# Kernel optimization log

Measured on AMD Instinct MI355X. Metric: run time of the kernel, lower is better.

Reference implementation:

```python
import jax, jax.numpy as jnp
import numpy as np

B, C, H, W = 1024, 256, 19, 19
CH, CV = 32, 48  # c_head, c_val
B_AVG = 9.0


def setup_inputs() -> dict:
    key = jax.random.key(0)
    ks = jax.random.split(key, 14)
    s = 0.05
    d = {}
    d["x"] = jax.random.normal(ks[0], (B, C, H, W), jnp.float32)
    d["conv_w"] = jax.random.normal(ks[1], (CH, C), jnp.float32) * s  # 1x1 conv, no bias
    d["fc1_w"] = jax.random.normal(ks[2], (CV, 3 * CH), jnp.float32) * s
    d["fc1_b"] = jax.random.normal(ks[3], (CV,), jnp.float32) * s
    d["fc2_w"] = jax.random.normal(ks[4], (1, CV), jnp.float32) * s
    d["fc2_b"] = jax.random.normal(ks[5], (1,), jnp.float32) * s
    d["fc3_w"] = jax.random.normal(ks[6], (CV, 3 * CH), jnp.float32) * s
    d["fc3_b"] = jax.random.normal(ks[7], (CV,), jnp.float32) * s
    d["sc_w"] = jax.random.normal(ks[8], (1, CV), jnp.float32) * s
    d["sc_b"] = jax.random.normal(ks[9], (1,), jnp.float32) * s
    d["fc4_w"] = jax.random.normal(ks[10], (CV, 3 * CH + 1), jnp.float32) * s
    d["fc4_b"] = jax.random.normal(ks[11], (CV,), jnp.float32) * s
    d["fc5_w"] = jax.random.normal(ks[12], (1, CV), jnp.float32) * s
    d["fc5_b"] = jax.random.normal(ks[13], (1,), jnp.float32) * s
    return d


def reference(x, conv_w, fc1_w, fc1_b, fc2_w, fc2_b, fc3_w, fc3_b,
              sc_w, sc_b, fc4_w, fc4_b, fc5_w, fc5_b):
    # 1x1 conv (bias=False) == channel-mixing matmul
    V = jnp.einsum('bchw,oc->bohw', x, conv_w)  # [B, CH, H, W]

    # GlobalPooling (value_head=False branch: real spatial max)
    mean1 = V.mean(axis=(2, 3))                         # [B, CH]
    mean2 = mean1 * ((V.shape[2] - B_AVG) / 10.0)       # [B, CH]
    mx = V.max(axis=(2, 3))                             # [B, CH]
    Vp = jnp.concatenate([mean1, mean2, mx], axis=1)    # [B, 3*CH]

    # game outcome head
    game_out = jnp.tanh(jax.nn.relu(Vp @ fc1_w.T + fc1_b) @ fc2_w.T + fc2_b)  # [B, 1]

    # scaling factor head
    scaling = jax.nn.relu(Vp @ fc3_w.T + fc3_b) @ sc_w.T + sc_b  # [B, 1]

    # distance logits: the original loops over 41 d values; here the d axis is batched.
    dvals = jnp.arange(-20, 21, dtype=jnp.float32)               # [41]
    base = Vp @ fc4_w[:, :-1].T + fc4_b                          # [B, CV]
    d_term = dvals[:, None] * fc4_w[:, -1][None, :]              # [41, CV]
    h = jax.nn.relu(base[:, None, :] + d_term[None, :, :])       # [B, 41, CV]
    logits = h @ fc5_w[0] + fc5_b[0]                             # [B, 41]

    probs = jax.nn.softmax(logits * scaling, axis=1)             # [B, 41]
    return (game_out, probs)
```

## Files before the change

### kernel.cpp

```cpp
#include <hip/hip_runtime.h>
#include <math.h>

#define C_IN   256
#define C_HEAD 32
#define HW     361
#define NTHR   384
#define CV     48
#define WSTR   264

typedef __attribute__((ext_vector_type(8))) short bf16x8;
typedef __attribute__((ext_vector_type(4))) float f32x4;

static __device__ __forceinline__ unsigned short f2bf(float f) {
    unsigned int u = __builtin_bit_cast(unsigned int, f);
    u += 0x7fffu + ((u >> 16) & 1u);
    return (unsigned short)(u >> 16);
}

__global__ __launch_bounds__(NTHR, 4) void vh_fused(
    const float* __restrict__ x,
    const float* __restrict__ conv_w,
    const float* __restrict__ fc1_w, const float* __restrict__ fc1_b,
    const float* __restrict__ fc2_w, const float* __restrict__ fc2_b,
    const float* __restrict__ fc3_w, const float* __restrict__ fc3_b,
    const float* __restrict__ sc_w,  const float* __restrict__ sc_b,
    const float* __restrict__ fc4_w, const float* __restrict__ fc4_b,
    const float* __restrict__ fc5_w, const float* __restrict__ fc5_b,
    float* __restrict__ out, int B)
{
    const int b    = blockIdx.x;
    const int tid  = threadIdx.x;
    const int wave = tid >> 6;
    const int lane = tid & 63;
    const int l15  = lane & 15;
    const int g    = lane >> 4;

    __shared__ __align__(16) unsigned short wtT[C_HEAD * WSTR];
    __shared__ float lds_psum[C_HEAD][6];
    __shared__ float lds_pmax[C_HEAD][6];
    __shared__ float vp[3 * C_HEAD];
    __shared__ float base_l[CV], dco_l[CV], f5_l[CV];

    for (int i = tid; i < C_HEAD * C_IN; i += NTHR) {
        int o = i >> 8, c = i & 255;
        wtT[o * WSTR + c] = f2bf(conv_w[i]);
    }
    __syncthreads();

    f32x4 acc[4][2];
    #pragma unroll
    for (int mi = 0; mi < 4; ++mi)
        #pragma unroll
        for (int n = 0; n < 2; ++n)
            acc[mi][n] = (f32x4){0.f, 0.f, 0.f, 0.f};

    const float* __restrict__ xb = x + (size_t)b * C_IN * HW;

    #pragma unroll
    for (int t = 0; t < 8; ++t) {
        bf16x8 wf[2];
        #pragma unroll
        for (int n = 0; n < 2; ++n)
            wf[n] = *(const bf16x8*)&wtT[(n * 16 + l15) * WSTR + t * 32 + g * 8];

        bf16x8 a[4];
        #pragma unroll
        for (int mi = 0; mi < 4; ++mi) {
            int p = wave * 64 + mi * 16 + l15;
            if (p >= HW) p = HW - 1;
            const float* xp = xb + (t * 32 + g * 8) * HW + p;
            float v[8];
            #pragma unroll
            for (int e = 0; e < 8; ++e) v[e] = xp[e * HW];
            bf16x8 f;
            #pragma unroll
            for (int e = 0; e < 8; ++e) f[e] = (short)f2bf(v[e]);
            a[mi] = f;
        }

        #pragma unroll
        for (int mi = 0; mi < 4; ++mi)
            #pragma unroll
            for (int n = 0; n < 2; ++n)
                acc[mi][n] = __builtin_amdgcn_mfma_f32_16x16x32_bf16(
                    a[mi], wf[n], acc[mi][n], 0, 0, 0);
    }

    float s[2]  = {0.f, 0.f};
    float mx[2] = {-3.0e38f, -3.0e38f};
    #pragma unroll
    for (int n = 0; n < 2; ++n) {
        #pragma unroll
        for (int mi = 0; mi < 4; ++mi) {
            #pragma unroll
            for (int r = 0; r < 4; ++r) {
                int pp = wave * 64 + mi * 16 + g * 4 + r;
                float v = acc[mi][n][r];
                if (pp < HW) { s[n] += v; mx[n] = fmaxf(mx[n], v); }
            }
        }
        s[n] += __shfl_xor(s[n], 16, 64);
        s[n] += __shfl_xor(s[n], 32, 64);
        mx[n] = fmaxf(mx[n], __shfl_xor(mx[n], 16, 64));
        mx[n] = fmaxf(mx[n], __shfl_xor(mx[n], 32, 64));
    }
    if (lane < 32) {
        lds_psum[lane][wave] = (lane < 16) ? s[0] : s[1];
        lds_pmax[lane][wave] = (lane < 16) ? mx[0] : mx[1];
    }
    __syncthreads();

    if (tid < C_HEAD) {
        float ss = 0.f, mm = -3.0e38f;
        #pragma unroll
        for (int w = 0; w < 6; ++w) { ss += lds_psum[tid][w]; mm = fmaxf(mm, lds_pmax[tid][w]); }
        float mean1 = ss * (1.0f / (float)HW);
        vp[tid]              = mean1;
        vp[C_HEAD + tid]     = mean1 * ((19.0f - 9.0f) * 0.1f);
        vp[2 * C_HEAD + tid] = mm;
    }
    __syncthreads();

    if (wave == 0) {
        const int j = lane;
        float h1 = 0.f, h3 = 0.f;
        if (j < CV) {
            float a1 = fc1_b[j], a3 = fc3_b[j], a4 = fc4_b[j];
            #pragma unroll
            for (int k = 0; k < 96; ++k) {
                float v = vp[k];
                a1 = fmaf(v, fc1_w[j * 96 + k], a1);
                a3 = fmaf(v, fc3_w[j * 96 + k], a3);
                a4 = fmaf(v, fc4_w[j * 97 + k], a4);
            }
            h1 = fmaxf(a1, 0.f) * fc2_w[j];
            h3 = fmaxf(a3, 0.f) * sc_w[j];
            base_l[j] = a4;
            dco_l[j]  = fc4_w[j * 97 + 96];
            f5_l[j]   = fc5_w[j];
        }
        float s1 = h1, s3 = h3;
        #pragma unroll
        for (int off = 32; off > 0; off >>= 1) {
            s1 += __shfl_xor(s1, off, 64);
            s3 += __shfl_xor(s3, off, 64);
        }
        float game = tanhf(s1 + fc2_b[0]);
        float scal = s3 + sc_b[0];
        if (lane == 0) out[b] = game;

        float z = -3.0e38f;
        if (lane < 41) {
            float dval = (float)(lane - 20);
            float lg = fc5_b[0];
            #pragma unroll
            for (int jj = 0; jj < CV; ++jj) {
                float t2 = fmaf(dval, dco_l[jj], base_l[jj]);
                t2 = fmaxf(t2, 0.f);
                lg = fmaf(t2, f5_l[jj], lg);
            }
            z = lg * scal;
        }
        float mz = z;
        #pragma unroll
        for (int off = 32; off > 0; off >>= 1) mz = fmaxf(mz, __shfl_xor(mz, off, 64));
        float e = (lane < 41) ? expf(z - mz) : 0.f;
        float se = e;
        #pragma unroll
        for (int off = 32; off > 0; off >>= 1) se += __shfl_xor(se, off, 64);
        if (lane < 41) out[B + b * 41 + lane] = e / se;
    }
}

extern "C" void kernel_launch(void* const* d_in, const int* in_sizes, int n_in,
                              void* d_out, int out_size, void* d_ws, size_t ws_size,
                              hipStream_t stream) {
    const float* x      = (const float*)d_in[0];
    const float* conv_w = (const float*)d_in[1];
    const float* fc1_w  = (const float*)d_in[2];
    const float* fc1_b  = (const float*)d_in[3];
    const float* fc2_w  = (const float*)d_in[4];
    const float* fc2_b  = (const float*)d_in[5];
    const float* fc3_w  = (const float*)d_in[6];
    const float* fc3_b  = (const float*)d_in[7];
    const float* sc_w   = (const float*)d_in[8];
    const float* sc_b   = (const float*)d_in[9];
    const float* fc4_w  = (const float*)d_in[10];
    const float* fc4_b  = (const float*)d_in[11];
    const float* fc5_w  = (const float*)d_in[12];
    const float* fc5_b  = (const float*)d_in[13];
    float* out = (float*)d_out;

    int B = in_sizes[0] / (C_IN * HW);

    vh_fused<<<dim3(B), dim3(NTHR), 0, stream>>>(
        x, conv_w, fc1_w, fc1_b, fc2_w, fc2_b, fc3_w, fc3_b,
        sc_w, sc_b, fc4_w, fc4_b, fc5_w, fc5_b, out, B);
}
```

Before: 111.6 us.

## Stage x chunks through double-buffered LDS with coalesced float4 loads

Replaces the strided per-lane global gathers of x with coalesced float4 loads of 32-channel chunks. The loaded values are converted to bf16 and stored into a double-buffered, padded LDS tile, and the MFMA A fragments are then read from LDS. The next chunk's global loads are issued before the current chunk's MFMAs to overlap memory with compute. This adds about 46KB of LDS per block and lowers the occupancy hint from 4 to 3 blocks per CU, which may reduce latency hiding.

```diff
diff --git a/kernel.cpp b/kernel.cpp
--- a/kernel.cpp
+++ b/kernel.cpp
@@ -7,6 +7,10 @@
 #define NTHR   384
 #define CV     48
 #define WSTR   264
+#define PSTR   364
+#define CCHUNK 32
+#define QUADS  2888
+#define NCHUNK 8
 
 typedef __attribute__((ext_vector_type(8))) short bf16x8;
 typedef __attribute__((ext_vector_type(4))) float f32x4;
@@ -17,7 +21,7 @@
     return (unsigned short)(u >> 16);
 }
 
-__global__ __launch_bounds__(NTHR, 4) void vh_fused(
+__global__ __launch_bounds__(NTHR, 3) void vh_fused(
     const float* __restrict__ x,
     const float* __restrict__ conv_w,
     const float* __restrict__ fc1_w, const float* __restrict__ fc1_b,
@@ -36,6 +40,7 @@
     const int g    = lane >> 4;
 
     __shared__ __align__(16) unsigned short wtT[C_HEAD * WSTR];
+    __shared__ __align__(16) unsigned short xs[2][CCHUNK * PSTR];
     __shared__ float lds_psum[C_HEAD][6];
     __shared__ float lds_pmax[C_HEAD][6];
     __shared__ float vp[3 * C_HEAD];
@@ -45,7 +50,49 @@
         int o = i >> 8, c = i & 255;
         wtT[o * WSTR + c] = f2bf(conv_w[i]);
     }
-    __syncthreads();
+
+    const float* __restrict__ xb = x + (size_t)b * (C_IN * HW);
+
+    float4 vreg[8];
+
+    auto loadq = [&](int q) {
+        #pragma unroll
+        for (int itv = 0; itv < 8; ++itv) {
+            int it = itv * NTHR + tid;
+            if (it < QUADS)
+                vreg[itv] = *(const float4*)(xb + q * (CCHUNK * HW) + it * 4);
+        }
+    };
+
+    auto writeq = [&](int buf) {
+        #pragma unroll
+        for (int itv = 0; itv < 8; ++itv) {
+            int it = itv * NTHR + tid;
+            if (it < QUADS) {
+                int fl = it * 4;
+                int cl = (int)__umulhi((unsigned)fl, 11897417u);
+                int p0 = fl - cl * 361;
+                float4 v = vreg[itv];
+                unsigned short h0 = f2bf(v.x), h1 = f2bf(v.y),
+                               h2 = f2bf(v.z), h3 = f2bf(v.w);
+                if (p0 <= 357) {
+                    unsigned int lo = (unsigned)h0 | ((unsigned)h1 << 16);
+                    unsigned int hi = (unsigned)h2 | ((unsigned)h3 << 16);
+                    *(uint2*)&xs[buf][cl * PSTR + p0 + (cl & 3)] = make_uint2(lo, hi);
+                } else {
+                    unsigned short hh[4] = {h0, h1, h2, h3};
+                    #pragma unroll
+                    for (int i2 = 0; i2 < 4; ++i2) {
+                        int p = p0 + i2;
+                        if (p < HW)
+                            xs[buf][cl * PSTR + p + (cl & 3)] = hh[i2];
+                        else
+                            xs[buf][(cl + 1) * PSTR + (p - HW) + ((cl + 1) & 3)] = hh[i2];
+                    }
+                }
+            }
+        }
+    };
 
     f32x4 acc[4][2];
     #pragma unroll
@@ -54,36 +101,34 @@
         for (int n = 0; n < 2; ++n)
             acc[mi][n] = (f32x4){0.f, 0.f, 0.f, 0.f};
 
-    const float* __restrict__ xb = x + (size_t)b * C_IN * HW;
-
-    #pragma unroll
-    for (int t = 0; t < 8; ++t) {
+    loadq(0);
+    writeq(0);
+
+    for (int q = 0; q < NCHUNK; ++q) {
+        __syncthreads();
+        if (q < NCHUNK - 1) loadq(q + 1);
+
         bf16x8 wf[2];
         #pragma unroll
         for (int n = 0; n < 2; ++n)
-            wf[n] = *(const bf16x8*)&wtT[(n * 16 + l15) * WSTR + t * 32 + g * 8];
-
-        bf16x8 a[4];
+            wf[n] = *(const bf16x8*)&wtT[(n * 16 + l15) * WSTR + q * 32 + g * 8];
+
+        const unsigned short* xc = xs[q & 1];
         #pragma unroll
         for (int mi = 0; mi < 4; ++mi) {
             int p = wave * 64 + mi * 16 + l15;
             if (p >= HW) p = HW - 1;
-            const float* xp = xb + (t * 32 + g * 8) * HW + p;
-            float v[8];
-            #pragma unroll
-            for (int e = 0; e < 8; ++e) v[e] = xp[e * HW];
-            bf16x8 f;
-            #pragma unroll
-            for (int e = 0; e < 8; ++e) f[e] = (short)f2bf(v[e]);
-            a[mi] = f;
-        }
-
-        #pragma unroll
-        for (int mi = 0; mi < 4; ++mi)
-            #pragma unroll
-            for (int n = 0; n < 2; ++n)
-                acc[mi][n] = __builtin_amdgcn_mfma_f32_16x16x32_bf16(
-                    a[mi], wf[n], acc[mi][n], 0, 0, 0);
+            bf16x8 a;
+            #pragma unroll
+            for (int e = 0; e < 8; ++e) {
+                int cl = g * 8 + e;
+                a[e] = (short)xc[cl * PSTR + p + (e & 3)];
+            }
+            acc[mi][0] = __builtin_amdgcn_mfma_f32_16x16x32_bf16(a, wf[0], acc[mi][0], 0, 0, 0);
+            acc[mi][1] = __builtin_amdgcn_mfma_f32_16x16x32_bf16(a, wf[1], acc[mi][1], 0, 0, 0);
+        }
+
+        if (q < NCHUNK - 1) writeq((q + 1) & 1);
     }
 
     float s[2]  = {0.f, 0.f};
```

Measured after the change: 141.3 us. 26.5% more time.

## Double-buffer global x loads in registers to overlap with MFMA compute

Applied to the files above, without the earlier changes.

Global loads of x are now software-pipelined across two register banks, so the loads for channel tile t+1 are issued before the bf16 conversion and MFMAs for tile t. Per-lane base offsets are precomputed once, and the bf16 packing is done explicitly into uint4 words. To make room for the extra 32 live float registers, the occupancy hint in launch_bounds drops from 4 to 3 blocks per CU. The trade is more memory-level parallelism per wave against fewer resident waves to hide latency.

```diff
diff --git a/kernel.cpp b/kernel.cpp
--- a/kernel.cpp
+++ b/kernel.cpp
@@ -17,7 +17,7 @@
     return (unsigned short)(u >> 16);
 }
 
-__global__ __launch_bounds__(NTHR, 4) void vh_fused(
+__global__ __launch_bounds__(NTHR, 3) void vh_fused(
     const float* __restrict__ x,
     const float* __restrict__ conv_w,
     const float* __restrict__ fc1_w, const float* __restrict__ fc1_b,
@@ -54,36 +54,52 @@
         for (int n = 0; n < 2; ++n)
             acc[mi][n] = (f32x4){0.f, 0.f, 0.f, 0.f};
 
-    const float* __restrict__ xb = x + (size_t)b * C_IN * HW;
-
+    const float* __restrict__ xb = x + (size_t)b * (C_IN * HW);
+
+    unsigned labase[4];
+    #pragma unroll
+    for (int mi = 0; mi < 4; ++mi) {
+        int p = wave * 64 + mi * 16 + l15;
+        if (p >= HW) p = HW - 1;
+        labase[mi] = (unsigned)(g * 8 * HW + p);
+    }
+
+    float rawA[32], rawB[32];
+
+    auto issue = [&](int t, float (&bank)[32]) {
+        #pragma unroll
+        for (int mi = 0; mi < 4; ++mi)
+            #pragma unroll
+            for (int e = 0; e < 8; ++e)
+                bank[mi * 8 + e] = xb[labase[mi] + (unsigned)((t * 32 + e) * HW)];
+    };
+
+    auto step = [&](int t, float (&bank)[32]) {
+        bf16x8 wf0 = *(const bf16x8*)&wtT[(      l15) * WSTR + t * 32 + g * 8];
+        bf16x8 wf1 = *(const bf16x8*)&wtT[(16 + l15) * WSTR + t * 32 + g * 8];
+        #pragma unroll
+        for (int mi = 0; mi < 4; ++mi) {
+            uint4 u;
+            u.x = (unsigned)f2bf(bank[mi*8+0]) | ((unsigned)f2bf(bank[mi*8+1]) << 16);
+            u.y = (unsigned)f2bf(bank[mi*8+2]) | ((unsigned)f2bf(bank[mi*8+3]) << 16);
+            u.z = (unsigned)f2bf(bank[mi*8+4]) | ((unsigned)f2bf(bank[mi*8+5]) << 16);
+            u.w = (unsigned)f2bf(bank[mi*8+6]) | ((unsigned)f2bf(bank[mi*8+7]) << 16);
+            bf16x8 a = __builtin_bit_cast(bf16x8, u);
+            acc[mi][0] = __builtin_amdgcn_mfma_f32_16x16x32_bf16(a, wf0, acc[mi][0], 0, 0, 0);
+            acc[mi][1] = __builtin_amdgcn_mfma_f32_16x16x32_bf16(a, wf1, acc[mi][1], 0, 0, 0);
+        }
+    };
+
+    issue(0, rawA);
     #pragma unroll
     for (int t = 0; t < 8; ++t) {
-        bf16x8 wf[2];
-        #pragma unroll
-        for (int n = 0; n < 2; ++n)
-            wf[n] = *(const bf16x8*)&wtT[(n * 16 + l15) * WSTR + t * 32 + g * 8];
-
-        bf16x8 a[4];
-        #pragma unroll
-        for (int mi = 0; mi < 4; ++mi) {
-            int p = wave * 64 + mi * 16 + l15;
-            if (p >= HW) p = HW - 1;
-            const float* xp = xb + (t * 32 + g * 8) * HW + p;
-            float v[8];
-            #pragma unroll
-            for (int e = 0; e < 8; ++e) v[e] = xp[e * HW];
-            bf16x8 f;
-            #pragma unroll
-            for (int e = 0; e < 8; ++e) f[e] = (short)f2bf(v[e]);
-            a[mi] = f;
-        }
-
-        #pragma unroll
-        for (int mi = 0; mi < 4; ++mi)
-            #pragma unroll
-            for (int n = 0; n < 2; ++n)
-                acc[mi][n] = __builtin_amdgcn_mfma_f32_16x16x32_bf16(
-                    a[mi], wf[n], acc[mi][n], 0, 0, 0);
+        if ((t & 1) == 0) {
+            if (t < 7) issue(t + 1, rawB);
+            step(t, rawA);
+        } else {
+            if (t < 7) issue(t + 1, rawA);
+            step(t, rawB);
+        }
     }
 
     float s[2]  = {0.f, 0.f};
```

Result: slower. 117.4 us (+5.1%).
